# Optimization experiments

Measured on AMD Instinct MI355X. Metric: run time of the kernel, lower is better.

## Reference

```python
import jax, jax.numpy as jnp
import numpy as np

# The four fixed 2x2 patterns from the original module
PATTERNS = jnp.array([[[1, 2], [0, 0]],
                      [[0, 1], [0, 2]],
                      [[0, 0], [2, 1]],
                      [[2, 0], [1, 0]]], dtype=jnp.int32)


def setup_inputs() -> dict:
    key = jax.random.key(0)
    k1, k2 = jax.random.split(key)
    b, c, w, h = 32, 3, 1024, 1024
    x = jax.random.normal(k1, (b, c, w, h), dtype=jnp.float32)
    initmask = jax.random.randint(k2, (b, 1, w // 2, h // 2), 0, 4, dtype=jnp.int64)
    return {"x": x, "initmask": initmask}


def reference(x, initmask):
    b, c, w, h = x.shape
    # gather pattern per 2x2 block: (b, w/2, h/2, 2, 2)
    fm = PATTERNS[initmask[:, 0]]
    # interleave block dims back into full resolution: (b, 1, w, h)
    fm = fm.transpose(0, 1, 3, 2, 4).reshape(b, 1, w, h)
    mask1 = jnp.broadcast_to((fm == 1).astype(x.dtype), x.shape)
    mask2 = jnp.broadcast_to((fm == 2).astype(x.dtype), x.shape)
    return (mask1, mask2)
```

## Files before the change

### kernel.cpp

```cpp
#include <hip/hip_runtime.h>


#define BB 32
#define CC 3
#define WW 1024
#define HH 1024
#define WM (WW / 2)
#define HM (HH / 2)
#define J2 (HM / 2)

__global__ __launch_bounds__(256) void masksampling_kernel(const int* __restrict__ im,
                                                           float* __restrict__ out) {
    const unsigned tid = blockIdx.x * 256u + threadIdx.x;
    const unsigned j2 = tid & (J2 - 1);
    const unsigned i  = (tid >> 8) & (WM - 1);
    const unsigned b  = tid >> 17;

    const int2 m2 = ((const int2*)im)[(b * WM + i) * J2 + j2];
    const unsigned PACK = 0x12608409u;
    const unsigned s0 = (unsigned)m2.x * 8u;
    const unsigned s1 = (unsigned)m2.y * 8u;

    float4* out1 = (float4*)out;
    float4* out2 = out1 + (BB * CC * WW * HH) / 4;

    #pragma unroll
    for (int di = 0; di < 2; ++di) {
        const unsigned v0 = (PACK >> (s0 + di * 4 + 0)) & 3u;
        const unsigned v1 = (PACK >> (s0 + di * 4 + 2)) & 3u;
        const unsigned v2 = (PACK >> (s1 + di * 4 + 0)) & 3u;
        const unsigned v3 = (PACK >> (s1 + di * 4 + 2)) & 3u;
        const float4 f1 = make_float4(v0 == 1u ? 1.f : 0.f, v1 == 1u ? 1.f : 0.f,
                                      v2 == 1u ? 1.f : 0.f, v3 == 1u ? 1.f : 0.f);
        const float4 f2 = make_float4(v0 == 2u ? 1.f : 0.f, v1 == 2u ? 1.f : 0.f,
                                      v2 == 2u ? 1.f : 0.f, v3 == 2u ? 1.f : 0.f);
        const unsigned r = 2u * i + (unsigned)di;
        #pragma unroll
        for (int c = 0; c < CC; ++c) {
            const unsigned off = ((b * CC + c) * WW + r) * (HH / 4) + j2;
            out1[off] = f1;
            out2[off] = f2;
        }
    }
}

extern "C" void kernel_launch(void* const* d_in, const int* in_sizes, int n_in,
                              void* d_out, int out_size, void* d_ws, size_t ws_size,
                              hipStream_t stream) {
    const int* im = (const int*)d_in[1];
    float* out = (float*)d_out;
    const int total = BB * WM * J2;
    masksampling_kernel<<<total / 256, 256, 0, stream>>>(im, out);
}
```

Before: 961.8 us.

## Map one thread per output float4 with bitmask pattern lookup

Restructures the grid so each thread writes exactly one float4 to each of the two outputs, instead of one thread writing twelve float4s across channels and rows. Writes become fully linear in thread index, and the pattern decode uses precomputed equality bitmasks in place of a packed-value compare. The cost is twelve times more threads and each mask element being reloaded once per channel and row, though those reloads should hit in cache.

```diff
diff --git a/kernel.cpp b/kernel.cpp
--- a/kernel.cpp
+++ b/kernel.cpp
@@ -1,47 +1,36 @@
 #include <hip/hip_runtime.h>
 
 
-#define BB 32
-#define CC 3
-#define WW 1024
-#define HH 1024
-#define WM (WW / 2)
-#define HM (HH / 2)
-#define J2 (HM / 2)
+#define N_F4_PER_OUT 25165824u
 
 __global__ __launch_bounds__(256) void masksampling_kernel(const int* __restrict__ im,
                                                            float* __restrict__ out) {
-    const unsigned tid = blockIdx.x * 256u + threadIdx.x;
-    const unsigned j2 = tid & (J2 - 1);
-    const unsigned i  = (tid >> 8) & (WM - 1);
-    const unsigned b  = tid >> 17;
+    const unsigned t = blockIdx.x * 256u + threadIdx.x;
+    const unsigned j  = t & 255u;
+    const unsigned r  = (t >> 8) & 1023u;
+    const unsigned bc = t >> 18;
+    const unsigned b  = bc / 3u;
 
-    const int2 m2 = ((const int2*)im)[(b * WM + i) * J2 + j2];
-    const unsigned PACK = 0x12608409u;
-    const unsigned s0 = (unsigned)m2.x * 8u;
-    const unsigned s1 = (unsigned)m2.y * 8u;
+    const int2 m2 = ((const int2*)im)[b * 131072u + (r >> 1) * 256u + j];
 
-    float4* out1 = (float4*)out;
-    float4* out2 = out1 + (BB * CC * WW * HH) / 4;
+    const unsigned base = (r & 1u) * 2u;
+    const unsigned s0 = (unsigned)m2.x * 4u + base;
+    const unsigned s1 = (unsigned)m2.y * 4u + base;
 
-    #pragma unroll
-    for (int di = 0; di < 2; ++di) {
-        const unsigned v0 = (PACK >> (s0 + di * 4 + 0)) & 3u;
-        const unsigned v1 = (PACK >> (s0 + di * 4 + 2)) & 3u;
-        const unsigned v2 = (PACK >> (s1 + di * 4 + 0)) & 3u;
-        const unsigned v3 = (PACK >> (s1 + di * 4 + 2)) & 3u;
-        const float4 f1 = make_float4(v0 == 1u ? 1.f : 0.f, v1 == 1u ? 1.f : 0.f,
-                                      v2 == 1u ? 1.f : 0.f, v3 == 1u ? 1.f : 0.f);
-        const float4 f2 = make_float4(v0 == 2u ? 1.f : 0.f, v1 == 2u ? 1.f : 0.f,
-                                      v2 == 2u ? 1.f : 0.f, v3 == 2u ? 1.f : 0.f);
-        const unsigned r = 2u * i + (unsigned)di;
-        #pragma unroll
-        for (int c = 0; c < CC; ++c) {
-            const unsigned off = ((b * CC + c) * WW + r) * (HH / 4) + j2;
-            out1[off] = f1;
-            out2[off] = f2;
-        }
-    }
+    const unsigned EQ1 = 0x4821u, EQ2 = 0x1482u;
+    const float4 f1 = make_float4((float)((EQ1 >> s0) & 1u),
+                                  (float)((EQ1 >> (s0 + 1u)) & 1u),
+                                  (float)((EQ1 >> s1) & 1u),
+                                  (float)((EQ1 >> (s1 + 1u)) & 1u));
+    const float4 f2 = make_float4((float)((EQ2 >> s0) & 1u),
+                                  (float)((EQ2 >> (s0 + 1u)) & 1u),
+                                  (float)((EQ2 >> s1) & 1u),
+                                  (float)((EQ2 >> (s1 + 1u)) & 1u));
+
+    float4* o1 = (float4*)out;
+    float4* o2 = o1 + N_F4_PER_OUT;
+    o1[t] = f1;
+    o2[t] = f2;
 }
 
 extern "C" void kernel_launch(void* const* d_in, const int* in_sizes, int n_in,
@@ -49,6 +38,5 @@
                               hipStream_t stream) {
     const int* im = (const int*)d_in[1];
     float* out = (float*)d_out;
-    const int total = BB * WM * J2;
-    masksampling_kernel<<<total / 256, 256, 0, stream>>>(im, out);
+    masksampling_kernel<<<N_F4_PER_OUT / 256, 256, 0, stream>>>(im, out);
 }
```

After: 940.6 us. -2.2%, faster.
